# Performance work log

Hardware: AMD Instinct MI355X
Metric: run time of the kernel (lower is better)

## Reference

```python
import jax, jax.numpy as jnp
import numpy as np

B, C, H, W = 16, 256, 128, 128
RED = 16  # reduction -> hidden = C // RED = 16


def setup_inputs() -> dict:
    key = jax.random.key(0)
    k = jax.random.split(key, 5)
    hid = C // RED
    return {
        "x": jax.random.normal(k[0], (B, C, H, W), dtype=jnp.float32),
        "w1": jax.random.normal(k[1], (hid, C), dtype=jnp.float32) * 0.05,
        "b1": jax.random.normal(k[2], (hid,), dtype=jnp.float32) * 0.05,
        "w2": jax.random.normal(k[3], (C, hid), dtype=jnp.float32) * 0.05,
        "b2": jax.random.normal(k[4], (C,), dtype=jnp.float32) * 0.05,
    }


def reference(x, w1, b1, w2, b2):
    # Global average pool over H, W -> [B, C]
    y = jnp.mean(x, axis=(2, 3))
    # 2-layer MLP (nn.Linear: y @ W.T + b) + sigmoid -> per-channel gates [B, C]
    h = jax.nn.relu(y @ w1.T + b1)
    s = jax.nn.sigmoid(h @ w2.T + b2)
    # Faithful to the original loop: only batch element 0 gets scaled by s[0].
    return x.at[0].multiply(s[0][:, None, None])
```

## Files before the change

### kernel.cpp

```cpp
#include <hip/hip_runtime.h>
#include <math.h>

#define HW    16384
#define CCH   256
#define HID   16

__global__ void se_pool(const float* __restrict__ x, float* __restrict__ y) {
    const int c = blockIdx.x;
    const float4* p = (const float4*)(x + (size_t)c * HW);
    float sum = 0.f;
    for (int i = threadIdx.x; i < HW / 4; i += blockDim.x) {
        float4 v = p[i];
        sum += (v.x + v.y) + (v.z + v.w);
    }
    #pragma unroll
    for (int off = 32; off > 0; off >>= 1)
        sum += __shfl_down(sum, off, 64);
    __shared__ float wsum[4];
    const int lane = threadIdx.x & 63;
    const int wave = threadIdx.x >> 6;
    if (lane == 0) wsum[wave] = sum;
    __syncthreads();
    if (threadIdx.x == 0) {
        float s = (wsum[0] + wsum[1]) + (wsum[2] + wsum[3]);
        y[c] = s * (1.0f / (float)HW);
    }
}

__global__ void se_mlp(const float* __restrict__ y,
                       const float* __restrict__ w1, const float* __restrict__ b1,
                       const float* __restrict__ w2, const float* __restrict__ b2,
                       float* __restrict__ s) {
    __shared__ float ysh[CCH];
    __shared__ float h[HID];
    const int t = threadIdx.x;
    ysh[t] = y[t];
    __syncthreads();
    if (t < HID) {
        float acc = b1[t];
        const float* wr = w1 + t * CCH;
        #pragma unroll 8
        for (int c = 0; c < CCH; ++c) acc = fmaf(ysh[c], wr[c], acc);
        h[t] = fmaxf(acc, 0.f);
    }
    __syncthreads();
    float acc = b2[t];
    const float* wr2 = w2 + t * HID;
    #pragma unroll
    for (int j = 0; j < HID; ++j) acc = fmaf(h[j], wr2[j], acc);
    s[t] = 1.0f / (1.0f + __expf(-acc));
}

__global__ void se_scale(const float* __restrict__ x, const float* __restrict__ s,
                         float* __restrict__ out) {
    const float4* __restrict__ xin = (const float4*)x;
    float4* __restrict__ o = (float4*)out;
    const size_t n4 = (size_t)16 * CCH * (HW / 4);
    const size_t b0 = (size_t)CCH * (HW / 4);
    size_t i = (size_t)blockIdx.x * blockDim.x + threadIdx.x;
    const size_t stride = (size_t)gridDim.x * blockDim.x;
    for (; i < n4; i += stride) {
        float4 v = xin[i];
        if (i < b0) {
            const float g = s[i >> 12];
            v.x *= g; v.y *= g; v.z *= g; v.w *= g;
        }
        o[i] = v;
    }
}

extern "C" void kernel_launch(void* const* d_in, const int* in_sizes, int n_in,
                              void* d_out, int out_size, void* d_ws, size_t ws_size,
                              hipStream_t stream) {
    const float* x  = (const float*)d_in[0];
    const float* w1 = (const float*)d_in[1];
    const float* b1 = (const float*)d_in[2];
    const float* w2 = (const float*)d_in[3];
    const float* b2 = (const float*)d_in[4];
    float* out = (float*)d_out;

    float* y = (float*)d_ws;
    float* s = y + CCH;

    se_pool<<<CCH, 256, 0, stream>>>(x, y);
    se_mlp<<<1, 256, 0, stream>>>(y, w1, b1, w2, b2, s);
    se_scale<<<16384, 256, 0, stream>>>(x, s, out);
}
```

Measured before the change: 452.4 us.

## Fuse SE pool, MLP and scale into one cooperative kernel with overlapped copy

Merges the three launches into one cooperative kernel of 1024 blocks that uses grid syncs. Batch 0 pooling is split across 4 blocks per channel. While block 0 computes the MLP gates, all blocks copy batches 1-15 to the output with nontemporal loads and stores. After the second grid sync they scale batch 0. This removes launch gaps and hides the serial MLP behind the bulk copy, at the cost of two grid-wide barriers and a reliance on cooperative launch residency.

```diff
diff --git a/kernel.cpp b/kernel.cpp
--- a/kernel.cpp
+++ b/kernel.cpp
@@ -1,71 +1,93 @@
 #include <hip/hip_runtime.h>
+#include <hip/hip_cooperative_groups.h>
 #include <math.h>
+
+namespace cg = cooperative_groups;
 
 #define HW    16384
 #define CCH   256
 #define HID   16
+#define NBLK  1024
+#define NTHR  256
+#define BPC   (NBLK / CCH)
 
-__global__ void se_pool(const float* __restrict__ x, float* __restrict__ y) {
-    const int c = blockIdx.x;
-    const float4* p = (const float4*)(x + (size_t)c * HW);
-    float sum = 0.f;
-    for (int i = threadIdx.x; i < HW / 4; i += blockDim.x) {
-        float4 v = p[i];
-        sum += (v.x + v.y) + (v.z + v.w);
+typedef float f4 __attribute__((ext_vector_type(4)));
+
+__global__ __launch_bounds__(NTHR, 4) void se_fused(
+        const float* __restrict__ x,
+        const float* __restrict__ w1, const float* __restrict__ b1,
+        const float* __restrict__ w2, const float* __restrict__ b2,
+        float* __restrict__ out, float* __restrict__ ws) {
+    cg::grid_group grid = cg::this_grid();
+    const int bid = blockIdx.x;
+    const int t   = threadIdx.x;
+    float* part = ws;
+    float* svec = ws + NBLK;
+
+    {
+        const int c = bid >> 2;
+        const int q = bid & (BPC - 1);
+        const f4* p = (const f4*)(x + (size_t)c * HW) + (size_t)q * (HW / 4 / BPC);
+        float sum = 0.f;
+        #pragma unroll
+        for (int i = 0; i < (HW / 4 / BPC) / NTHR; ++i) {
+            f4 v = p[(size_t)i * NTHR + t];
+            sum += (v.x + v.y) + (v.z + v.w);
+        }
+        #pragma unroll
+        for (int off = 32; off > 0; off >>= 1)
+            sum += __shfl_down(sum, off, 64);
+        __shared__ float wsum[NTHR / 64];
+        if ((t & 63) == 0) wsum[t >> 6] = sum;
+        __syncthreads();
+        if (t == 0) part[bid] = (wsum[0] + wsum[1]) + (wsum[2] + wsum[3]);
     }
-    #pragma unroll
-    for (int off = 32; off > 0; off >>= 1)
-        sum += __shfl_down(sum, off, 64);
-    __shared__ float wsum[4];
-    const int lane = threadIdx.x & 63;
-    const int wave = threadIdx.x >> 6;
-    if (lane == 0) wsum[wave] = sum;
-    __syncthreads();
-    if (threadIdx.x == 0) {
-        float s = (wsum[0] + wsum[1]) + (wsum[2] + wsum[3]);
-        y[c] = s * (1.0f / (float)HW);
+    grid.sync();
+
+    if (bid == 0) {
+        __shared__ float ysh[CCH];
+        __shared__ float h[HID];
+        float acc0 = 0.f;
+        #pragma unroll
+        for (int k = 0; k < BPC; ++k) acc0 += part[t * BPC + k];
+        ysh[t] = acc0 * (1.0f / (float)HW);
+        __syncthreads();
+        if (t < HID) {
+            float acc = b1[t];
+            const float* wr = w1 + t * CCH;
+            #pragma unroll 8
+            for (int c = 0; c < CCH; ++c) acc = fmaf(ysh[c], wr[c], acc);
+            h[t] = fmaxf(acc, 0.f);
+        }
+        __syncthreads();
+        float acc = b2[t];
+        const float* wr2 = w2 + t * HID;
+        #pragma unroll
+        for (int j = 0; j < HID; ++j) acc = fmaf(h[j], wr2[j], acc);
+        svec[t] = 1.0f / (1.0f + __expf(-acc));
     }
-}
+    {
+        const size_t base4 = (size_t)CCH * (HW / 4);
+        const size_t n4    = 15 * base4;
+        const f4* __restrict__ xin = (const f4*)x + base4;
+        f4* __restrict__ o = (f4*)out + base4;
+        for (size_t i = (size_t)bid * NTHR + t; i < n4; i += (size_t)NBLK * NTHR) {
+            f4 v = __builtin_nontemporal_load(xin + i);
+            __builtin_nontemporal_store(v, o + i);
+        }
+    }
+    grid.sync();
 
-__global__ void se_mlp(const float* __restrict__ y,
-                       const float* __restrict__ w1, const float* __restrict__ b1,
-                       const float* __restrict__ w2, const float* __restrict__ b2,
-                       float* __restrict__ s) {
-    __shared__ float ysh[CCH];
-    __shared__ float h[HID];
-    const int t = threadIdx.x;
-    ysh[t] = y[t];
-    __syncthreads();
-    if (t < HID) {
-        float acc = b1[t];
-        const float* wr = w1 + t * CCH;
-        #pragma unroll 8
-        for (int c = 0; c < CCH; ++c) acc = fmaf(ysh[c], wr[c], acc);
-        h[t] = fmaxf(acc, 0.f);
-    }
-    __syncthreads();
-    float acc = b2[t];
-    const float* wr2 = w2 + t * HID;
-    #pragma unroll
-    for (int j = 0; j < HID; ++j) acc = fmaf(h[j], wr2[j], acc);
-    s[t] = 1.0f / (1.0f + __expf(-acc));
-}
-
-__global__ void se_scale(const float* __restrict__ x, const float* __restrict__ s,
-                         float* __restrict__ out) {
-    const float4* __restrict__ xin = (const float4*)x;
-    float4* __restrict__ o = (float4*)out;
-    const size_t n4 = (size_t)16 * CCH * (HW / 4);
-    const size_t b0 = (size_t)CCH * (HW / 4);
-    size_t i = (size_t)blockIdx.x * blockDim.x + threadIdx.x;
-    const size_t stride = (size_t)gridDim.x * blockDim.x;
-    for (; i < n4; i += stride) {
-        float4 v = xin[i];
-        if (i < b0) {
-            const float g = s[i >> 12];
+    {
+        const size_t b0 = (size_t)CCH * (HW / 4);
+        const f4* __restrict__ xin = (const f4*)x;
+        f4* __restrict__ o = (f4*)out;
+        for (size_t i = (size_t)bid * NTHR + t; i < b0; i += (size_t)NBLK * NTHR) {
+            f4 v = xin[i];
+            const float g = svec[i >> 12];
             v.x *= g; v.y *= g; v.z *= g; v.w *= g;
+            __builtin_nontemporal_store(v, o + i);
         }
-        o[i] = v;
     }
 }
 
@@ -78,11 +100,10 @@
     const float* w2 = (const float*)d_in[3];
     const float* b2 = (const float*)d_in[4];
     float* out = (float*)d_out;
+    float* ws  = (float*)d_ws;
 
-    float* y = (float*)d_ws;
-    float* s = y + CCH;
-
-    se_pool<<<CCH, 256, 0, stream>>>(x, y);
-    se_mlp<<<1, 256, 0, stream>>>(y, w1, b1, w2, b2, s);
-    se_scale<<<16384, 256, 0, stream>>>(x, s, out);
+    void* args[] = {(void*)&x, (void*)&w1, (void*)&b1, (void*)&w2, (void*)&b2,
+                    (void*)&out, (void*)&ws};
+    hipLaunchCooperativeKernel((const void*)se_fused, dim3(NBLK), dim3(NTHR),
+                               args, 0, stream);
 }
```

Measured after the change: 629.8 us. 39.2% more time.
